# Kernel optimization log

Hardware: AMD Instinct MI355X
Metric: run time of the kernel (lower is better)

The kernel has to match this reference:

```python
import jax, jax.numpy as jnp
import numpy as np

NUM_Q = 4
BETA = 0.25
TEMP = 0.1
EPS = 1e-12


def setup_inputs() -> dict:
    key = jax.random.key(0)
    k1, k2, k3, k4 = jax.random.split(key, 4)
    N, D, NE, K = 32768, 256, 256, 4096
    return {
        "x": jax.random.normal(k1, (N, D), dtype=jnp.float32),
        "codebooks": jax.random.normal(k2, (NUM_Q, NE, D), dtype=jnp.float32) * 0.02,
        "pair_idx1": jax.random.randint(k3, (K,), 0, N),
        "pair_idx2": jax.random.randint(k4, (K,), 0, N),
    }


def _quantize(residual, codebook):
    # squared L2 cdist: ||r||^2 - 2 r.e + ||e||^2  -> [N, n_e]
    d2 = (jnp.sum(residual * residual, axis=1, keepdims=True)
          - 2.0 * residual @ codebook.T
          + jnp.sum(codebook * codebook, axis=1))
    idx = jnp.argmin(d2, axis=1)                      # [N]
    q = codebook[idx]                                 # gather [N, D]
    sg = jax.lax.stop_gradient
    loss = jnp.mean((sg(q) - residual) ** 2) + BETA * jnp.mean((q - sg(residual)) ** 2)
    x_res = residual + sg(q - residual)               # straight-through
    return x_res, loss, idx


def _outer_contrastive(feat, i1, i2):
    # L2-normalize rows (torch F.normalize, eps clamp)
    xn = feat * jax.lax.rsqrt(jnp.sum(feat * feat, axis=1, keepdims=True) + EPS)
    pos = jnp.sum(xn[i1] * xn[i2], axis=1) / TEMP     # [K]
    sim = (xn[i1] @ xn.T) / TEMP                      # [K, N]
    # CE with positive at sim[:, i2]; excluded-positive column equals pos,
    # so logsumexp over [pos, negatives] == logsumexp over the full row.
    return jnp.mean(jax.nn.logsumexp(sim, axis=1) - pos)


def reference(x, codebooks, pair_idx1, pair_idx2):
    residual = x
    x_q = jnp.zeros_like(x)
    vq_losses, outer_losses, all_idx = [], [], []
    for q in range(NUM_Q):
        outer_losses.append(_outer_contrastive(residual, pair_idx1, pair_idx2))
        x_res, loss, idx = _quantize(residual, codebooks[q])
        residual = residual - x_res
        x_q = x_q + x_res
        vq_losses.append(loss)
        all_idx.append(idx)
    mean_loss = jnp.mean(jnp.stack(vq_losses))
    return (x_q, mean_loss, jnp.stack(outer_losses), jnp.stack(all_idx, axis=-1))
```

## Files before the change

### kernel.cpp

```cpp
#include <hip/hip_runtime.h>

#define N_ROWS 32768
#define DIM    256
#define NE     256
#define KP     4096
#define NQ     4
#define ND     8388608
#define RESCORE_MARGIN 2e-4f

typedef short short8 __attribute__((ext_vector_type(8)));
typedef unsigned short ushort8v __attribute__((ext_vector_type(8)));
typedef float f32x4  __attribute__((ext_vector_type(4)));

__device__ inline float bf2f(unsigned short u) {
  return __uint_as_float(((unsigned)u) << 16);
}
__device__ inline unsigned short f2bf(float f) {
  unsigned u = __float_as_uint(f);
  u += 0x7fffu + ((u >> 16) & 1u);
  return (unsigned short)(u >> 16);
}
__device__ inline float fexp2(float x) { return __builtin_amdgcn_exp2f(x); }

__device__ inline size_t chunkIdx(int row, int j) {
  return (size_t)(((row >> 4) * 8 + (j >> 2)) * 64 + ((j & 3) << 4) + (row & 15));
}

__global__ __launch_bounds__(256) void prep0_kernel(
    const float* __restrict__ x,
    unsigned short* __restrict__ Xnp, float* __restrict__ rnorm,
    unsigned short* __restrict__ rHp, unsigned short* __restrict__ rLp) {
  __shared__ float ldsNr[16 * 260];
  __shared__ float ssl[16];
  const int tid = threadIdx.x, wave = tid >> 6, lane = tid & 63;
  const int t = blockIdx.x;
#pragma unroll
  for (int rr = 0; rr < 4; ++rr) {
    const int rl = wave * 4 + rr;
    const int row = t * 16 + rl;
    float4 v = ((const float4*)(x + (size_t)row * DIM))[lane];
    float ss = v.x * v.x + v.y * v.y + v.z * v.z + v.w * v.w;
#pragma unroll
    for (int m = 1; m < 64; m <<= 1) ss += __shfl_xor(ss, m, 64);
    *(float4*)(&ldsNr[rl * 260 + lane * 4]) = v;
    if (lane == 0) { ssl[rl] = ss; rnorm[row] = ss; }
  }
  __syncthreads();
  const int l16 = lane & 15, quad = lane >> 4;
  const float sc = rsqrtf(ssl[l16] + 1e-12f);
#pragma unroll
  for (int ff = 0; ff < 2; ++ff) {
    const int f = wave * 2 + ff;
    const float* p = &ldsNr[l16 * 260 + f * 32 + quad * 8];
    float4 u0 = *(const float4*)(p);
    float4 u1 = *(const float4*)(p + 4);
    float vv[8] = {u0.x, u0.y, u0.z, u0.w, u1.x, u1.y, u1.z, u1.w};
    ushort8v h, l, xn;
#pragma unroll
    for (int u = 0; u < 8; ++u) {
      h[u] = f2bf(vv[u]); l[u] = f2bf(vv[u] - bf2f(h[u])); xn[u] = f2bf(vv[u] * sc);
    }
    const size_t c = ((size_t)(t * 8 + f) * 64 + lane) * 8;
    *(ushort8v*)(rHp + c) = h;
    *(ushort8v*)(rLp + c) = l;
    *(ushort8v*)(Xnp + c) = xn;
  }
}

__global__ __launch_bounds__(256) void cbnorm_kernel(
    const float* __restrict__ cb, float* __restrict__ cbn) {
  const int wave = threadIdx.x >> 6, lane = threadIdx.x & 63;
  const int e = blockIdx.x * 4 + wave;
  float4 v = ((const float4*)(cb + (size_t)e * DIM))[lane];
  float ss = v.x * v.x + v.y * v.y + v.z * v.z + v.w * v.w;
#pragma unroll
  for (int m = 1; m < 64; m <<= 1) ss += __shfl_xor(ss, m, 64);
  if (lane == 0) cbn[e] = ss;
}

__global__ __launch_bounds__(256) void cbsplit_kernel(
    const float* __restrict__ cb, unsigned short* __restrict__ cbHp,
    unsigned short* __restrict__ cbLp) {
  const int p = blockIdx.x * 256 + threadIdx.x;
  const int stage = p >> 13, ps = p & 8191;
  const int l16 = ps & 15, quad = (ps >> 4) & 3, kf = (ps >> 6) & 7, et = ps >> 9;
  const int e = et * 16 + l16, k0 = kf * 32 + quad * 8;
  const float* src = cb + ((size_t)(stage * NE + e)) * DIM + k0;
  float4 v0 = ((const float4*)src)[0], v1 = ((const float4*)src)[1];
  float vv[8] = {v0.x, v0.y, v0.z, v0.w, v1.x, v1.y, v1.z, v1.w};
  ushort8v h, l;
#pragma unroll
  for (int i = 0; i < 8; ++i) {
    h[i] = f2bf(vv[i]); l[i] = f2bf(vv[i] - bf2f(h[i]));
  }
  *(ushort8v*)(cbHp + (size_t)p * 8) = h;
  *(ushort8v*)(cbLp + (size_t)p * 8) = l;
}

__global__ __launch_bounds__(256) void gather_pos_kernel(
    const unsigned short* __restrict__ Xnp, const int* __restrict__ i1,
    const int* __restrict__ i2, unsigned short* __restrict__ Qgp,
    float* __restrict__ pos, float* __restrict__ ssum) {
  if (blockIdx.x < 16) ssum[blockIdx.x * 256 + threadIdx.x] = 0.0f;
  const int wave = threadIdx.x >> 6, lane = threadIdx.x & 63;
  const int k = blockIdx.x * 4 + wave;
  const int a = i1[k], b = i2[k];
  const int j2 = lane >> 1, off = (lane & 1) * 4;
  ushort4 va = *(const ushort4*)(Xnp + chunkIdx(a, j2) * 8 + off);
  ushort4 vb = *(const ushort4*)(Xnp + chunkIdx(b, j2) * 8 + off);
  *(ushort4*)(Qgp + chunkIdx(k, j2) * 8 + off) = va;
  float d = bf2f(va.x) * bf2f(vb.x) + bf2f(va.y) * bf2f(vb.y) +
            bf2f(va.z) * bf2f(vb.z) + bf2f(va.w) * bf2f(vb.w);
#pragma unroll
  for (int m = 1; m < 64; m <<= 1) d += __shfl_xor(d, m, 64);
  if (lane == 0) pos[k] = d * 10.0f;
}


__device__ __forceinline__ void sim_body(
    int sid, unsigned short* ldsB,
    const unsigned short* __restrict__ Qgp,
    const unsigned short* __restrict__ Xnp,
    float* __restrict__ s_sum) {
  const int tid  = threadIdx.x;
  const int lane = tid & 63;
  const int wave = tid >> 6;
  const int quad = lane >> 4;
  const int l16  = lane & 15;
  const int bx = sid & 31;
  const int by = sid >> 5;
  const int qt0  = bx * 8 + wave * 2;
  const int qbase = bx * 128 + wave * 32;

  short8 a[2][8];
#pragma unroll
  for (int t = 0; t < 2; ++t)
#pragma unroll
    for (int f = 0; f < 8; ++f)
      a[t][f] = *(const short8*)(Qgp + ((size_t)(((qt0 + t) * 8 + f) * 64 + lane)) * 8);

  float s[2][4] = {};
  const float C1 = 14.4269504088896341f;
  const unsigned short* bsrc = Xnp + (size_t)(by * 32) * 4096;

  auto stageB = [&](int g) {
    const unsigned short* src = bsrc + (size_t)g * 4096 + wave * 1024 + lane * 8;
#pragma unroll
    for (int p = 0; p < 2; ++p)
      __builtin_amdgcn_global_load_lds(
          (const __attribute__((address_space(1))) unsigned int*)(src + p * 512),
          (__attribute__((address_space(3))) unsigned int*)(&ldsB[wave * 1024 + p * 512]),
          16, 0, 0);
  };

  stageB(0);
  for (int g = 0; g < 32; ++g) {
    asm volatile("s_waitcnt vmcnt(0)" ::: "memory");
    __builtin_amdgcn_s_barrier();
    __builtin_amdgcn_sched_barrier(0);
    short8 b[8];
#pragma unroll
    for (int f = 0; f < 8; ++f)
      b[f] = *(const short8*)(&ldsB[f * 512 + lane * 8]);
    asm volatile("s_waitcnt lgkmcnt(0)" ::: "memory");
    __builtin_amdgcn_s_barrier();
    __builtin_amdgcn_sched_barrier(0);
    if (g + 1 < 32) stageB(g + 1);

    f32x4 acc0[2] = {{0.f, 0.f, 0.f, 0.f}, {0.f, 0.f, 0.f, 0.f}};
    f32x4 acc1[2] = {{0.f, 0.f, 0.f, 0.f}, {0.f, 0.f, 0.f, 0.f}};
#pragma unroll
    for (int f = 0; f < 4; ++f)
#pragma unroll
      for (int t = 0; t < 2; ++t) {
        acc0[t] = __builtin_amdgcn_mfma_f32_16x16x32_bf16(a[t][f], b[f], acc0[t], 0, 0, 0);
        acc1[t] = __builtin_amdgcn_mfma_f32_16x16x32_bf16(a[t][f + 4], b[f + 4], acc1[t], 0, 0, 0);
      }
#pragma unroll
    for (int t = 0; t < 2; ++t) {
      f32x4 m = acc0[t] + acc1[t];
#pragma unroll
      for (int i = 0; i < 4; ++i)
        s[t][i] += fexp2(fmaf(m[i], C1, -C1));
    }
  }
#pragma unroll
  for (int m = 1; m < 16; m <<= 1)
#pragma unroll
    for (int t = 0; t < 2; ++t)
#pragma unroll
      for (int i = 0; i < 4; ++i) s[t][i] += __shfl_xor(s[t][i], m, 64);
  if (l16 == 0) {
#pragma unroll
    for (int t = 0; t < 2; ++t)
#pragma unroll
      for (int i = 0; i < 4; ++i)
        atomicAdd(&s_sum[qbase + t * 16 + quad * 4 + i], s[t][i]);
  }
}

__device__ __forceinline__ void argmin_body(
    int aid, char* smem,
    const float* __restrict__ xin, const float* __restrict__ resid,
    const float* __restrict__ cb,
    const unsigned short* __restrict__ cbHp, const unsigned short* __restrict__ cbLp,
    const float* __restrict__ cbn, const float* __restrict__ rnorm,
    const unsigned short* __restrict__ rHp, const unsigned short* __restrict__ rLp,
    int* __restrict__ outIdx, int stage) {
  float (*sV1)[32] = (float(*)[32])(smem);
  float (*sV2)[32] = (float(*)[32])(smem + 512);
  int   (*sIx)[32] = (int(*)[32])(smem + 1024);
  int*   sIdx      = (int*)(smem + 1536);
  int*   sFlag     = (int*)(smem + 1664);
  const int tid  = threadIdx.x;
  const int lane = tid & 63;
  const int wave = tid >> 6;
  const int quad = lane >> 4;
  const int l16  = lane & 15;
  const int rbase = aid * 32;
  const int t0 = aid * 2;
  const float* __restrict__ src = (stage == 0) ? xin : resid;

  f32x4 acc4[2][4];
#pragma unroll
  for (int rt = 0; rt < 2; ++rt)
#pragma unroll
    for (int ct = 0; ct < 4; ++ct) acc4[rt][ct] = (f32x4){0.f, 0.f, 0.f, 0.f};

  auto loadA = [&](int kf, short8 (&aH)[2], short8 (&aL)[2]) {
#pragma unroll
    for (int rt = 0; rt < 2; ++rt) {
      const size_t off = ((size_t)(((t0 + rt) * 8 + kf) * 64 + lane)) * 8;
      aH[rt] = *(const short8*)(rHp + off);
      aL[rt] = *(const short8*)(rLp + off);
    }
  };
  auto loadBc = [&](int kf, short8 (&bH)[4], short8 (&bL)[4]) {
#pragma unroll
    for (int ct = 0; ct < 4; ++ct) {
      const size_t boff = ((size_t)(((wave * 4 + ct) * 8 + kf) * 64 + lane)) * 8;
      bH[ct] = *(const short8*)(cbHp + boff);
      bL[ct] = *(const short8*)(cbLp + boff);
    }
  };
  auto computeK = [&](short8 (&aH)[2], short8 (&aL)[2], short8 (&bH)[4],
                      short8 (&bL)[4]) {
#pragma unroll
    for (int ct = 0; ct < 4; ++ct)
#pragma unroll
      for (int rt = 0; rt < 2; ++rt) {
        acc4[rt][ct] = __builtin_amdgcn_mfma_f32_16x16x32_bf16(aL[rt], bH[ct], acc4[rt][ct], 0, 0, 0);
        acc4[rt][ct] = __builtin_amdgcn_mfma_f32_16x16x32_bf16(aH[rt], bL[ct], acc4[rt][ct], 0, 0, 0);
        acc4[rt][ct] = __builtin_amdgcn_mfma_f32_16x16x32_bf16(aH[rt], bH[ct], acc4[rt][ct], 0, 0, 0);
      }
  };

  short8 aH0[2], aL0[2], bH0[4], bL0[4], aH1[2], aL1[2], bH1[4], bL1[4];
  loadA(0, aH0, aL0); loadBc(0, bH0, bL0);
  for (int kf = 0; kf < 8; kf += 2) {
    loadA(kf + 1, aH1, aL1); loadBc(kf + 1, bH1, bL1);
    computeK(aH0, aL0, bH0, bL0);
    if (kf + 2 < 8) { loadA(kf + 2, aH0, aL0); loadBc(kf + 2, bH0, bL0); }
    computeK(aH1, aL1, bH1, bL1);
  }

  float cbe[4];
#pragma unroll
  for (int ct = 0; ct < 4; ++ct) cbe[ct] = cbn[(wave * 4 + ct) * 16 + l16];
#pragma unroll
  for (int rt = 0; rt < 2; ++rt) {
    float b1[4], b2[4]; int e1[4];
#pragma unroll
    for (int i = 0; i < 4; ++i) { b1[i] = 3.4e38f; b2[i] = 3.4e38f; e1[i] = 0; }
#pragma unroll
    for (int ct = 0; ct < 4; ++ct) {
      const int e = (wave * 4 + ct) * 16 + l16;
#pragma unroll
      for (int i = 0; i < 4; ++i) {
        const float v = fmaf(-2.0f, acc4[rt][ct][i], cbe[ct]);
        if (v < b1[i]) { b2[i] = b1[i]; b1[i] = v; e1[i] = e; }
        else if (v < b2[i]) b2[i] = v;
      }
    }
#pragma unroll
    for (int m = 1; m < 16; m <<= 1) {
#pragma unroll
      for (int i = 0; i < 4; ++i) {
        const float o1 = __shfl_xor(b1[i], m, 64);
        const float o2 = __shfl_xor(b2[i], m, 64);
        const int   oe = __shfl_xor(e1[i], m, 64);
        if (o1 < b1[i] || (o1 == b1[i] && oe < e1[i])) {
          b2[i] = fminf(b1[i], o2); b1[i] = o1; e1[i] = oe;
        } else {
          b2[i] = fminf(b2[i], o1);
        }
      }
    }
    if (l16 == 0) {
#pragma unroll
      for (int i = 0; i < 4; ++i) {
        const int r = rt * 16 + quad * 4 + i;
        sV1[wave][r] = b1[i]; sV2[wave][r] = b2[i]; sIx[wave][r] = e1[i];
      }
    }
  }
  __syncthreads();
  if (tid < 32) {
    float v1 = 3.4e38f, v2 = 3.4e38f; int ix = 0;
#pragma unroll
    for (int w = 0; w < 4; ++w) {
      const float a1 = sV1[w][tid], a2 = sV2[w][tid];
      const int ae = sIx[w][tid];
      if (a1 < v1) { v2 = fminf(v1, a2); v1 = a1; ix = ae; }
      else { v2 = fminf(v2, fminf(a1, a2)); }
    }
    sIdx[tid] = ix;
    sFlag[tid] = (v2 - v1 < RESCORE_MARGIN) ? 1 : 0;
  }
  __syncthreads();

  for (int rr = 0; rr < 8; ++rr) {
    const int r = wave * 8 + rr;
    if (sFlag[r]) {
      const int row = rbase + r;
      const float* rrow = src + (size_t)row * DIM;
      float d[4] = {0.f, 0.f, 0.f, 0.f};
      for (int kb = 0; kb < 64; ++kb) {
        const float4 rv = ((const float4*)rrow)[kb];
#pragma unroll
        for (int j = 0; j < 4; ++j) {
          const float4 cv = ((const float4*)(cb + (size_t)(lane + 64 * j) * DIM))[kb];
          d[j] = fmaf(rv.x, cv.x, d[j]);
          d[j] = fmaf(rv.y, cv.y, d[j]);
          d[j] = fmaf(rv.z, cv.z, d[j]);
          d[j] = fmaf(rv.w, cv.w, d[j]);
        }
      }
      const float rn = rnorm[row];
      float bv = 3.4e38f; int be = 0;
#pragma unroll
      for (int j = 0; j < 4; ++j) {
        const int e = lane + 64 * j;
        const float v = (rn - 2.0f * d[j]) + cbn[e];
        if (v < bv) { bv = v; be = e; }
      }
#pragma unroll
      for (int m = 1; m < 64; m <<= 1) {
        const float vo = __shfl_xor(bv, m, 64);
        const int   eo = __shfl_xor(be, m, 64);
        if (vo < bv || (vo == bv && eo < be)) { bv = vo; be = eo; }
      }
      if (lane == 0) sIdx[r] = be;
    }
  }
  __syncthreads();
  if (tid < 32) outIdx[rbase + tid] = sIdx[tid];
}

__global__ __launch_bounds__(256, 2) void sim_argmin_kernel(
    const unsigned short* __restrict__ Qgp, const unsigned short* __restrict__ Xnp,
    float* __restrict__ s_sum,
    const float* __restrict__ xin, const float* __restrict__ resid,
    const float* __restrict__ cb,
    const unsigned short* __restrict__ cbHp, const unsigned short* __restrict__ cbLp,
    const float* __restrict__ cbn, const float* __restrict__ rnorm,
    const unsigned short* __restrict__ rHp, const unsigned short* __restrict__ rLp,
    int* __restrict__ outIdx, int stage) {
  __shared__ unsigned short smem[4096];
  const int g = blockIdx.x;
  const int q3 = g / 3, r3 = g - q3 * 3;
  if (r3 < 2) {
    sim_body(q3 * 2 + r3, smem, Qgp, Xnp, s_sum);
  } else {
    argmin_body(q3, (char*)smem, xin, resid, cb, cbHp, cbLp, cbn, rnorm,
                rHp, rLp, outIdx, stage);
  }
}

__global__ __launch_bounds__(256) void lse_final_kernel(
    const float* __restrict__ s_sum, const float* __restrict__ pos,
    float* __restrict__ acc, int stage) {
  const int t = threadIdx.x;
  const int k = blockIdx.x * 256 + t;
  float v = 10.0f + __logf(s_sum[k]) - pos[k];
#pragma unroll
  for (int m = 1; m < 64; m <<= 1) v += __shfl_xor(v, m, 64);
  __shared__ float red[4];
  if ((t & 63) == 0) red[t >> 6] = v;
  __syncthreads();
  if (t == 0) atomicAdd(&acc[4 + stage], red[0] + red[1] + red[2] + red[3]);
}

__global__ __launch_bounds__(256) void update_kernel(
    const float* __restrict__ xin, float* __restrict__ resid,
    const float* __restrict__ cb, const int* __restrict__ idx,
    float* __restrict__ rnorm,
    unsigned short* __restrict__ rHp, unsigned short* __restrict__ rLp,
    unsigned short* __restrict__ Xnp,
    float* __restrict__ xq, float* __restrict__ idxf, float* __restrict__ acc,
    int stage) {
  __shared__ float ldsNr[16 * 260];
  __shared__ float ssl[16];
  __shared__ float sred[4];
  const int tid = threadIdx.x, wave = tid >> 6, lane = tid & 63;
  const int t = blockIdx.x;
  const float* __restrict__ src = (stage == 0) ? xin : resid;

  float msum = 0.f;
#pragma unroll
  for (int rr = 0; rr < 4; ++rr) {
    const int rl = wave * 4 + rr;
    const int row = t * 16 + rl;
    const int e = idx[row];
    float4 v = ((const float4*)(src + (size_t)row * DIM))[lane];
    float4 c = ((const float4*)(cb + (size_t)e * DIM))[lane];
    float4 nr = {v.x - c.x, v.y - c.y, v.z - c.z, v.w - c.w};
    float ss = nr.x * nr.x + nr.y * nr.y + nr.z * nr.z + nr.w * nr.w;
#pragma unroll
    for (int m = 1; m < 64; m <<= 1) ss += __shfl_xor(ss, m, 64);
    if (stage < 3) {
      ((float4*)(resid + (size_t)row * DIM))[lane] = nr;
      *(float4*)(&ldsNr[rl * 260 + lane * 4]) = nr;
      if (lane == 0) { ssl[rl] = ss; rnorm[row] = ss; }
    } else {
      float4 xv = ((const float4*)(xin + (size_t)row * DIM))[lane];
      ((float4*)(xq + (size_t)row * DIM))[lane] =
          (float4){xv.x - nr.x, xv.y - nr.y, xv.z - nr.z, xv.w - nr.w};
    }
    if (lane == 0) {
      idxf[(size_t)row * NQ + stage] = (float)e;
      msum += ss;
    }
  }
  if (lane == 0) sred[wave] = msum;
  __syncthreads();
  if (tid == 0) atomicAdd(&acc[0], sred[0] + sred[1] + sred[2] + sred[3]);

  if (stage < 3) {
    const int l16 = lane & 15, quad = lane >> 4;
    const float sc = rsqrtf(ssl[l16] + 1e-12f);
#pragma unroll
    for (int ff = 0; ff < 2; ++ff) {
      const int f = wave * 2 + ff;
      const float* p = &ldsNr[l16 * 260 + f * 32 + quad * 8];
      float4 u0 = *(const float4*)(p);
      float4 u1 = *(const float4*)(p + 4);
      float vv[8] = {u0.x, u0.y, u0.z, u0.w, u1.x, u1.y, u1.z, u1.w};
      ushort8v h, l, xn;
#pragma unroll
      for (int u = 0; u < 8; ++u) {
        h[u] = f2bf(vv[u]); l[u] = f2bf(vv[u] - bf2f(h[u])); xn[u] = f2bf(vv[u] * sc);
      }
      const size_t c = ((size_t)(t * 8 + f) * 64 + lane) * 8;
      *(ushort8v*)(rHp + c) = h;
      *(ushort8v*)(rLp + c) = l;
      *(ushort8v*)(Xnp + c) = xn;
    }
  }
}

__global__ void finalize_kernel(const float* __restrict__ acc, float* __restrict__ out) {
  const int t = threadIdx.x;
  if (t == 0) out[ND] = acc[0] * (1.25f / (4.0f * (float)ND));
  if (t < 4) out[ND + 1 + t] = acc[4 + t] * (1.0f / (float)KP);
}

extern "C" void kernel_launch(void* const* d_in, const int* in_sizes, int n_in,
                              void* d_out, int out_size, void* d_ws, size_t ws_size,
                              hipStream_t stream) {
  const float* x         = (const float*)d_in[0];
  const float* codebooks = (const float*)d_in[1];
  const int*   i1        = (const int*)d_in[2];
  const int*   i2        = (const int*)d_in[3];
  float* out = (float*)d_out;
  float* out_xq   = out;
  float* out_idxf = out + ND + 1 + NQ;

  char* w = (char*)d_ws;
  float*          resid = (float*)w;          w += (size_t)N_ROWS * DIM * 4;
  unsigned short* Xnp   = (unsigned short*)w; w += (size_t)N_ROWS * DIM * 2;
  unsigned short* rHp   = (unsigned short*)w; w += (size_t)N_ROWS * DIM * 2;
  unsigned short* rLp   = (unsigned short*)w; w += (size_t)N_ROWS * DIM * 2;
  float*          rnorm = (float*)w;          w += (size_t)N_ROWS * 4;
  unsigned short* Qgp   = (unsigned short*)w; w += (size_t)KP * DIM * 2;
  float*          pos   = (float*)w;          w += (size_t)KP * 4;
  float*          ssum  = (float*)w;          w += (size_t)KP * 4;
  float*          cbn   = (float*)w;          w += (size_t)NQ * NE * 4;
  unsigned short* cbHp  = (unsigned short*)w; w += (size_t)NQ * NE * DIM * 2;
  unsigned short* cbLp  = (unsigned short*)w; w += (size_t)NQ * NE * DIM * 2;
  float*          acc   = (float*)w;          w += 32;
  int*            sidx  = (int*)w;            w += (size_t)N_ROWS * 4;

  prep0_kernel<<<2048, 256, 0, stream>>>(x, Xnp, rnorm, rHp, rLp);
  cbnorm_kernel<<<256, 256, 0, stream>>>(codebooks, cbn);
  cbsplit_kernel<<<128, 256, 0, stream>>>(codebooks, cbHp, cbLp);
  hipMemsetAsync(acc, 0, 32, stream);
  for (int q = 0; q < NQ; ++q) {
    const float* cb = codebooks + (size_t)q * NE * DIM;
    gather_pos_kernel<<<1024, 256, 0, stream>>>(Xnp, i1, i2, Qgp, pos, ssum);
    sim_argmin_kernel<<<3072, 256, 0, stream>>>(
        Qgp, Xnp, ssum, x, resid, cb,
        cbHp + (size_t)q * NE * DIM, cbLp + (size_t)q * NE * DIM,
        cbn + q * NE, rnorm, rHp, rLp, sidx, q);
    lse_final_kernel<<<16, 256, 0, stream>>>(ssum, pos, acc, q);
    update_kernel<<<2048, 256, 0, stream>>>(
        x, resid, cb, sidx, rnorm, rHp, rLp, Xnp, out_xq, out_idxf, acc, q);
  }
  finalize_kernel<<<1, 64, 0, stream>>>(acc, out);
}
```

Before: 644.2 us.

## Fuse residual update into argmin blocks and double-buffer normalized features

Each argmin block now does the residual update itself right after choosing codewords: it writes the new residual, the hi/lo bf16 splits, the normalized bf16 features, the norms, the indices and the loss partials. This removes the separate update kernel, the index buffer round trip and one launch per stage. Sim blocks in the same launch still read the current normalized features, so those are double-buffered (XnpA/XnpB) to avoid a write-after-read race. In exchange, the argmin blocks get heavier and their update writes use the chunkIdx layout instead of an LDS transpose.

```diff
diff --git a/kernel.cpp b/kernel.cpp
--- a/kernel.cpp
+++ b/kernel.cpp
@@ -129,6 +129,7 @@
   const int l16  = lane & 15;
   const int bx = sid & 31;
   const int by = sid >> 5;
+
   const int qt0  = bx * 8 + wave * 2;
   const int qbase = bx * 128 + wave * 32;
 
@@ -199,19 +200,22 @@
   }
 }
 
-__device__ __forceinline__ void argmin_body(
+__device__ __forceinline__ void argmin_update_body(
     int aid, char* smem,
-    const float* __restrict__ xin, const float* __restrict__ resid,
+    const float* __restrict__ xin, float* __restrict__ resid,
     const float* __restrict__ cb,
     const unsigned short* __restrict__ cbHp, const unsigned short* __restrict__ cbLp,
-    const float* __restrict__ cbn, const float* __restrict__ rnorm,
-    const unsigned short* __restrict__ rHp, const unsigned short* __restrict__ rLp,
-    int* __restrict__ outIdx, int stage) {
+    const float* __restrict__ cbn, float* __restrict__ rnorm,
+    unsigned short* __restrict__ rHp, unsigned short* __restrict__ rLp,
+    unsigned short* __restrict__ XnpN,
+    float* __restrict__ xq, float* __restrict__ idxf, float* __restrict__ acc,
+    int stage) {
   float (*sV1)[32] = (float(*)[32])(smem);
   float (*sV2)[32] = (float(*)[32])(smem + 512);
   int   (*sIx)[32] = (int(*)[32])(smem + 1024);
   int*   sIdx      = (int*)(smem + 1536);
   int*   sFlag     = (int*)(smem + 1664);
+  float* sred      = (float*)(smem + 1792);
   const int tid  = threadIdx.x;
   const int lane = tid & 63;
   const int wave = tid >> 6;
@@ -354,26 +358,77 @@
     }
   }
   __syncthreads();
-  if (tid < 32) outIdx[rbase + tid] = sIdx[tid];
+
+  const int half = lane >> 5, j = lane & 31;
+  float msum = 0.0f;
+  for (int i = 0; i < 4; ++i) {
+    const int rr = i * 8 + wave * 2 + half;
+    const int row = rbase + rr;
+    const int e = sIdx[rr];
+    const float4* rp = (const float4*)(src + (size_t)row * DIM + j * 8);
+    float4 r0 = rp[0], r1 = rp[1];
+    const float4* qp = (const float4*)(cb + (size_t)e * DIM + j * 8);
+    float4 q0 = qp[0], q1 = qp[1];
+    float nr[8] = {r0.x - q0.x, r0.y - q0.y, r0.z - q0.z, r0.w - q0.w,
+                   r1.x - q1.x, r1.y - q1.y, r1.z - q1.z, r1.w - q1.w};
+    float ss = 0.f;
+#pragma unroll
+    for (int u = 0; u < 8; ++u) ss += nr[u] * nr[u];
+    if (stage == 3) {
+      const float4* xr = (const float4*)(xin + (size_t)row * DIM + j * 8);
+      float4 x0 = xr[0], x1 = xr[1];
+      float4* xp = (float4*)(xq + (size_t)row * DIM + j * 8);
+      xp[0] = (float4){x0.x - nr[0], x0.y - nr[1], x0.z - nr[2], x0.w - nr[3]};
+      xp[1] = (float4){x1.x - nr[4], x1.y - nr[5], x1.z - nr[6], x1.w - nr[7]};
+    }
+#pragma unroll
+    for (int m = 1; m < 32; m <<= 1) ss += __shfl_xor(ss, m, 64);
+    if (stage < 3) {
+      float4* rw = (float4*)(resid + (size_t)row * DIM + j * 8);
+      rw[0] = (float4){nr[0], nr[1], nr[2], nr[3]};
+      rw[1] = (float4){nr[4], nr[5], nr[6], nr[7]};
+      const float sc = rsqrtf(ss + 1e-12f);
+      ushort8v h, l, xn;
+#pragma unroll
+      for (int u = 0; u < 8; ++u) {
+        h[u] = f2bf(nr[u]); l[u] = f2bf(nr[u] - bf2f(h[u])); xn[u] = f2bf(nr[u] * sc);
+      }
+      const size_t c = chunkIdx(row, j) * 8;
+      *(ushort8v*)(rHp + c) = h;
+      *(ushort8v*)(rLp + c) = l;
+      *(ushort8v*)(XnpN + c) = xn;
+      if (j == 0) rnorm[row] = ss;
+    }
+    if (j == 0) {
+      idxf[(size_t)row * NQ + stage] = (float)e;
+      msum += ss;
+    }
+  }
+  msum += __shfl_xor(msum, 32, 64);
+  if (lane == 0) sred[wave] = msum;
+  __syncthreads();
+  if (tid == 0) atomicAdd(&acc[0], sred[0] + sred[1] + sred[2] + sred[3]);
 }
 
 __global__ __launch_bounds__(256, 2) void sim_argmin_kernel(
     const unsigned short* __restrict__ Qgp, const unsigned short* __restrict__ Xnp,
     float* __restrict__ s_sum,
-    const float* __restrict__ xin, const float* __restrict__ resid,
+    const float* __restrict__ xin, float* __restrict__ resid,
     const float* __restrict__ cb,
     const unsigned short* __restrict__ cbHp, const unsigned short* __restrict__ cbLp,
-    const float* __restrict__ cbn, const float* __restrict__ rnorm,
-    const unsigned short* __restrict__ rHp, const unsigned short* __restrict__ rLp,
-    int* __restrict__ outIdx, int stage) {
+    const float* __restrict__ cbn, float* __restrict__ rnorm,
+    unsigned short* __restrict__ rHp, unsigned short* __restrict__ rLp,
+    unsigned short* __restrict__ XnpN,
+    float* __restrict__ xq, float* __restrict__ idxf, float* __restrict__ acc,
+    int stage) {
   __shared__ unsigned short smem[4096];
   const int g = blockIdx.x;
   const int q3 = g / 3, r3 = g - q3 * 3;
   if (r3 < 2) {
     sim_body(q3 * 2 + r3, smem, Qgp, Xnp, s_sum);
   } else {
-    argmin_body(q3, (char*)smem, xin, resid, cb, cbHp, cbLp, cbn, rnorm,
-                rHp, rLp, outIdx, stage);
+    argmin_update_body(q3, (char*)smem, xin, resid, cb, cbHp, cbLp, cbn,
+                       rnorm, rHp, rLp, XnpN, xq, idxf, acc, stage);
   }
 }
 
@@ -389,74 +444,6 @@
   if ((t & 63) == 0) red[t >> 6] = v;
   __syncthreads();
   if (t == 0) atomicAdd(&acc[4 + stage], red[0] + red[1] + red[2] + red[3]);
-}
-
-__global__ __launch_bounds__(256) void update_kernel(
-    const float* __restrict__ xin, float* __restrict__ resid,
-    const float* __restrict__ cb, const int* __restrict__ idx,
-    float* __restrict__ rnorm,
-    unsigned short* __restrict__ rHp, unsigned short* __restrict__ rLp,
-    unsigned short* __restrict__ Xnp,
-    float* __restrict__ xq, float* __restrict__ idxf, float* __restrict__ acc,
-    int stage) {
-  __shared__ float ldsNr[16 * 260];
-  __shared__ float ssl[16];
-  __shared__ float sred[4];
-  const int tid = threadIdx.x, wave = tid >> 6, lane = tid & 63;
-  const int t = blockIdx.x;
-  const float* __restrict__ src = (stage == 0) ? xin : resid;
-
-  float msum = 0.f;
-#pragma unroll
-  for (int rr = 0; rr < 4; ++rr) {
-    const int rl = wave * 4 + rr;
-    const int row = t * 16 + rl;
-    const int e = idx[row];
-    float4 v = ((const float4*)(src + (size_t)row * DIM))[lane];
-    float4 c = ((const float4*)(cb + (size_t)e * DIM))[lane];
-    float4 nr = {v.x - c.x, v.y - c.y, v.z - c.z, v.w - c.w};
-    float ss = nr.x * nr.x + nr.y * nr.y + nr.z * nr.z + nr.w * nr.w;
-#pragma unroll
-    for (int m = 1; m < 64; m <<= 1) ss += __shfl_xor(ss, m, 64);
-    if (stage < 3) {
-      ((float4*)(resid + (size_t)row * DIM))[lane] = nr;
-      *(float4*)(&ldsNr[rl * 260 + lane * 4]) = nr;
-      if (lane == 0) { ssl[rl] = ss; rnorm[row] = ss; }
-    } else {
-      float4 xv = ((const float4*)(xin + (size_t)row * DIM))[lane];
-      ((float4*)(xq + (size_t)row * DIM))[lane] =
-          (float4){xv.x - nr.x, xv.y - nr.y, xv.z - nr.z, xv.w - nr.w};
-    }
-    if (lane == 0) {
-      idxf[(size_t)row * NQ + stage] = (float)e;
-      msum += ss;
-    }
-  }
-  if (lane == 0) sred[wave] = msum;
-  __syncthreads();
-  if (tid == 0) atomicAdd(&acc[0], sred[0] + sred[1] + sred[2] + sred[3]);
-
-  if (stage < 3) {
-    const int l16 = lane & 15, quad = lane >> 4;
-    const float sc = rsqrtf(ssl[l16] + 1e-12f);
-#pragma unroll
-    for (int ff = 0; ff < 2; ++ff) {
-      const int f = wave * 2 + ff;
-      const float* p = &ldsNr[l16 * 260 + f * 32 + quad * 8];
-      float4 u0 = *(const float4*)(p);
-      float4 u1 = *(const float4*)(p + 4);
-      float vv[8] = {u0.x, u0.y, u0.z, u0.w, u1.x, u1.y, u1.z, u1.w};
-      ushort8v h, l, xn;
-#pragma unroll
-      for (int u = 0; u < 8; ++u) {
-        h[u] = f2bf(vv[u]); l[u] = f2bf(vv[u] - bf2f(h[u])); xn[u] = f2bf(vv[u] * sc);
-      }
-      const size_t c = ((size_t)(t * 8 + f) * 64 + lane) * 8;
-      *(ushort8v*)(rHp + c) = h;
-      *(ushort8v*)(rLp + c) = l;
-      *(ushort8v*)(Xnp + c) = xn;
-    }
-  }
 }
 
 __global__ void finalize_kernel(const float* __restrict__ acc, float* __restrict__ out) {
@@ -478,7 +465,8 @@
 
   char* w = (char*)d_ws;
   float*          resid = (float*)w;          w += (size_t)N_ROWS * DIM * 4;
-  unsigned short* Xnp   = (unsigned short*)w; w += (size_t)N_ROWS * DIM * 2;
+  unsigned short* XnpA  = (unsigned short*)w; w += (size_t)N_ROWS * DIM * 2;
+  unsigned short* XnpB  = (unsigned short*)w; w += (size_t)N_ROWS * DIM * 2;
   unsigned short* rHp   = (unsigned short*)w; w += (size_t)N_ROWS * DIM * 2;
   unsigned short* rLp   = (unsigned short*)w; w += (size_t)N_ROWS * DIM * 2;
   float*          rnorm = (float*)w;          w += (size_t)N_ROWS * 4;
@@ -489,22 +477,22 @@
   unsigned short* cbHp  = (unsigned short*)w; w += (size_t)NQ * NE * DIM * 2;
   unsigned short* cbLp  = (unsigned short*)w; w += (size_t)NQ * NE * DIM * 2;
   float*          acc   = (float*)w;          w += 32;
-  int*            sidx  = (int*)w;            w += (size_t)N_ROWS * 4;
-
-  prep0_kernel<<<2048, 256, 0, stream>>>(x, Xnp, rnorm, rHp, rLp);
+
+  prep0_kernel<<<2048, 256, 0, stream>>>(x, XnpA, rnorm, rHp, rLp);
   cbnorm_kernel<<<256, 256, 0, stream>>>(codebooks, cbn);
   cbsplit_kernel<<<128, 256, 0, stream>>>(codebooks, cbHp, cbLp);
   hipMemsetAsync(acc, 0, 32, stream);
+  unsigned short* XnpCur = XnpA;
+  unsigned short* XnpNxt = XnpB;
   for (int q = 0; q < NQ; ++q) {
     const float* cb = codebooks + (size_t)q * NE * DIM;
-    gather_pos_kernel<<<1024, 256, 0, stream>>>(Xnp, i1, i2, Qgp, pos, ssum);
+    gather_pos_kernel<<<1024, 256, 0, stream>>>(XnpCur, i1, i2, Qgp, pos, ssum);
     sim_argmin_kernel<<<3072, 256, 0, stream>>>(
-        Qgp, Xnp, ssum, x, resid, cb,
+        Qgp, XnpCur, ssum, x, resid, cb,
         cbHp + (size_t)q * NE * DIM, cbLp + (size_t)q * NE * DIM,
-        cbn + q * NE, rnorm, rHp, rLp, sidx, q);
+        cbn + q * NE, rnorm, rHp, rLp, XnpNxt, out_xq, out_idxf, acc, q);
     lse_final_kernel<<<16, 256, 0, stream>>>(ssum, pos, acc, q);
-    update_kernel<<<2048, 256, 0, stream>>>(
-        x, resid, cb, sidx, rnorm, rHp, rLp, Xnp, out_xq, out_idxf, acc, q);
+    unsigned short* tmp = XnpCur; XnpCur = XnpNxt; XnpNxt = tmp;
   }
   finalize_kernel<<<1, 64, 0, stream>>>(acc, out);
 }
```

Measured after the change: 536.8 us. 1.2x faster.
